# Kernel optimization log

Hardware: AMD Instinct MI355X
Metric: run time of the kernel (lower is better)

Reference implementation:

```python
import jax, jax.numpy as jnp
import numpy as np

N = 50000
E = 800000
C_IN, C_HID, C_OUT = 128, 64, 1


def setup_inputs() -> dict:
    key = jax.random.key(0)
    ks = jax.random.split(key, 8)
    x = jax.random.normal(ks[0], (N, C_IN), dtype=jnp.float32)
    edge_index = jax.random.randint(ks[1], (2, E), 0, N, dtype=jnp.int64)
    # GCNConv linear params (glorot-ish scaling)
    W1 = jax.random.normal(ks[2], (C_IN, C_HID), dtype=jnp.float32) / np.sqrt(C_IN)
    b1 = jnp.zeros((C_HID,), dtype=jnp.float32)
    W2 = jax.random.normal(ks[3], (C_HID, C_HID), dtype=jnp.float32) / np.sqrt(C_HID)
    b2 = jnp.zeros((C_HID,), dtype=jnp.float32)
    W3 = jax.random.normal(ks[4], (C_HID, C_OUT), dtype=jnp.float32) / np.sqrt(C_HID)
    b3 = jnp.zeros((C_OUT,), dtype=jnp.float32)
    return {"x": x, "edge_index": edge_index, "W1": W1, "b1": b1,
            "W2": W2, "b2": b2, "W3": W3, "b3": b3}


def _gcn_norm(edge_index, num_nodes):
    # Add self-loops, compute symmetric normalization D^{-1/2} A D^{-1/2}
    loop = jnp.arange(num_nodes, dtype=edge_index.dtype)
    src = jnp.concatenate([edge_index[0], loop])  # message sources
    dst = jnp.concatenate([edge_index[1], loop])  # message targets
    ones = jnp.ones(src.shape[0], dtype=jnp.float32)
    deg = jax.ops.segment_sum(ones, dst, num_segments=num_nodes)
    dis = jnp.where(deg > 0, jax.lax.rsqrt(jnp.maximum(deg, 1.0)), 0.0)
    norm = dis[src] * dis[dst]  # [E+N]
    return src, dst, norm


def _gcn_conv(h, src, dst, norm, W, b, num_nodes):
    h = h @ W                                  # [N, C_out]
    msg = h[src] * norm[:, None]               # gather + scale, [E+N, C_out]
    out = jax.ops.segment_sum(msg, dst, num_segments=num_nodes)  # scatter-add
    return out + b


def reference(x, edge_index, W1, b1, W2, b2, W3, b3):
    num_nodes = x.shape[0]
    src, dst, norm = _gcn_norm(edge_index, num_nodes)
    leaky = lambda v: jnp.where(v >= 0, v, 0.01 * v)
    h = _gcn_conv(x, src, dst, norm, W1, b1, num_nodes)
    h = leaky(h)
    h = _gcn_conv(h, src, dst, norm, W2, b2, num_nodes)
    h = leaky(h)
    h = _gcn_conv(h, src, dst, norm, W3, b3, num_nodes)
    return h
```

## Files before the change

kernel.cpp:

```cpp
#include <hip/hip_runtime.h>

#define CIN 128
#define CHID 64
#define CSTRIDE 64

__device__ __forceinline__ float leaky(float v) { return v >= 0.f ? v : 0.01f * v; }
__device__ __forceinline__ float bcast(float v, int k) {
    return __int_as_float(__builtin_amdgcn_readlane(__float_as_int(v), k));
}
__device__ __forceinline__ void acc4(float4& a, const float4 v) {
    a.x += v.x; a.y += v.y; a.z += v.z; a.w += v.w;
}
__device__ __forceinline__ void xorred(float4& a) {
    a.x += __shfl_xor(a.x, 16, 64); a.y += __shfl_xor(a.y, 16, 64);
    a.z += __shfl_xor(a.z, 16, 64); a.w += __shfl_xor(a.w, 16, 64);
    a.x += __shfl_xor(a.x, 32, 64); a.y += __shfl_xor(a.y, 32, 64);
    a.z += __shfl_xor(a.z, 32, 64); a.w += __shfl_xor(a.w, 32, 64);
}

__global__ void k_deg(const int* __restrict__ dst, const int* __restrict__ src,
                      int* __restrict__ deg, unsigned short* __restrict__ csr,
                      int E, int nps, int N) {
    const int shard = blockIdx.x & 7;
    const int chunk = blockIdx.x >> 3;
    const int nchunks = gridDim.x >> 3;
    const int lo = shard * nps;
    const int hi = min(lo + nps, N);
    const int estride = nchunks * 256;
    for (int e = chunk * 256 + threadIdx.x; e < E; e += estride) {
        int d = dst[e];
        if (d >= lo && d < hi) {
            int slot = atomicAdd(&deg[d], 1);
            if (slot < CSTRIDE) csr[(d << 6) + slot] = (unsigned short)src[e];
        }
    }
}

__global__ __launch_bounds__(256) void k_gemm1(
    const float* __restrict__ x, const float* __restrict__ W,
    const int* __restrict__ deg, float* __restrict__ hp, int N) {
    const int wave = threadIdx.x >> 6, lane = threadIdx.x & 63;
    float w[CIN];
#pragma unroll
    for (int k = 0; k < CIN; ++k) w[k] = W[k * CHID + lane];
    const int stride = gridDim.x * 4;
    for (int n = blockIdx.x * 4 + wave; n < N; n += stride) {
        float x0 = x[(size_t)n * CIN + lane];
        float x1 = x[(size_t)n * CIN + 64 + lane];
        float acc0 = 0.f, acc1 = 0.f;
#pragma unroll
        for (int k = 0; k < 64; k += 2) {
            acc0 = fmaf(bcast(x0, k),     w[k],     acc0);
            acc1 = fmaf(bcast(x0, k + 1), w[k + 1], acc1);
        }
#pragma unroll
        for (int k = 0; k < 64; k += 2) {
            acc0 = fmaf(bcast(x1, k),     w[64 + k],     acc0);
            acc1 = fmaf(bcast(x1, k + 1), w[64 + k + 1], acc1);
        }
        float dn = rsqrtf((float)(deg[n] + 1));
        hp[(size_t)n * CHID + lane] = dn * (acc0 + acc1);
    }
}

__global__ __launch_bounds__(256) void kG1(
    const unsigned short* __restrict__ csr, const int* __restrict__ deg,
    const float* __restrict__ hp, const float* __restrict__ W2,
    const float* __restrict__ b1, float* __restrict__ hp2, int N) {
    const int wave = threadIdx.x >> 6, lane = threadIdx.x & 63;
    const int g = lane >> 4, sl = lane & 15;
    float w[CHID];
#pragma unroll
    for (int k = 0; k < CHID; ++k) w[k] = W2[k * CHID + lane];
    const float4 bb = ((const float4*)b1)[sl];
    const float4* __restrict__ hpq = (const float4*)hp;
    const int stride = gridDim.x * 4;
    const int n0 = blockIdx.x * 4 + wave;
    int d = 0, c0 = 0, c1 = 0, c2 = 0, c3 = 0;
    if (n0 < N) {
        d = deg[n0];
        int base = n0 << 6;
        c0 = csr[base + g];      c1 = csr[base + g + 4];
        c2 = csr[base + g + 8];  c3 = csr[base + g + 12];
    }
    for (int n = n0; n < N; n += stride) {
        const int n2 = n + stride;
        int dN = 0, e0 = 0, e1 = 0, e2 = 0, e3 = 0;
        if (n2 < N) {
            dN = deg[n2];
            int b2 = n2 << 6;
            e0 = csr[b2 + g];      e1 = csr[b2 + g + 4];
            e2 = csr[b2 + g + 8];  e3 = csr[b2 + g + 12];
        }
        const int dc = d, base = n << 6;
        float4 a0 = make_float4(0.f, 0.f, 0.f, 0.f), a1 = a0, a2 = a0, a3 = a0;
        if (g == 0) a0 = hpq[(size_t)n * 16 + sl];
        if (g < dc)      acc4(a0, hpq[(size_t)c0 * 16 + sl]);
        if (g + 4 < dc)  acc4(a1, hpq[(size_t)c1 * 16 + sl]);
        if (g + 8 < dc)  acc4(a2, hpq[(size_t)c2 * 16 + sl]);
        if (g + 12 < dc) acc4(a3, hpq[(size_t)c3 * 16 + sl]);
        for (int b = g + 16; b < dc; b += 16) {
            { int s = csr[base + b];      acc4(a0, hpq[(size_t)s * 16 + sl]); }
            if (b + 4 < dc)  { int s = csr[base + b + 4];  acc4(a1, hpq[(size_t)s * 16 + sl]); }
            if (b + 8 < dc)  { int s = csr[base + b + 8];  acc4(a2, hpq[(size_t)s * 16 + sl]); }
            if (b + 12 < dc) { int s = csr[base + b + 12]; acc4(a3, hpq[(size_t)s * 16 + sl]); }
        }
        acc4(a0, a1); acc4(a2, a3); acc4(a0, a2);
        xorred(a0);
        float dn = rsqrtf((float)(dc + 1));
        float4 gv;
        gv.x = leaky(dn * a0.x + bb.x);
        gv.y = leaky(dn * a0.y + bb.y);
        gv.z = leaky(dn * a0.z + bb.z);
        gv.w = leaky(dn * a0.w + bb.w);
        float acc0 = 0.f, acc1 = 0.f;
#pragma unroll
        for (int i = 0; i < 16; ++i) {
            acc0 = fmaf(bcast(gv.x, i), w[4 * i + 0], acc0);
            acc1 = fmaf(bcast(gv.y, i), w[4 * i + 1], acc1);
            acc0 = fmaf(bcast(gv.z, i), w[4 * i + 2], acc0);
            acc1 = fmaf(bcast(gv.w, i), w[4 * i + 3], acc1);
        }
        hp2[(size_t)n * CHID + lane] = dn * (acc0 + acc1);
        d = dN; c0 = e0; c1 = e1; c2 = e2; c3 = e3;
    }
}

__global__ __launch_bounds__(256) void kG2(
    const unsigned short* __restrict__ csr, const int* __restrict__ deg,
    const float* __restrict__ hp, const float* __restrict__ b2,
    const float* __restrict__ W3, float* __restrict__ hp3, int N) {
    const int wave = threadIdx.x >> 6, lane = threadIdx.x & 63;
    const int g = lane >> 4, sl = lane & 15;
    const float4 bb = ((const float4*)b2)[sl];
    const float4 w3 = ((const float4*)W3)[sl];
    const float4* __restrict__ hpq = (const float4*)hp;
    const int stride = gridDim.x * 4;
    const int n0 = blockIdx.x * 4 + wave;
    int d = 0, c0 = 0, c1 = 0, c2 = 0, c3 = 0;
    if (n0 < N) {
        d = deg[n0];
        int base = n0 << 6;
        c0 = csr[base + g];      c1 = csr[base + g + 4];
        c2 = csr[base + g + 8];  c3 = csr[base + g + 12];
    }
    for (int n = n0; n < N; n += stride) {
        const int n2 = n + stride;
        int dN = 0, e0 = 0, e1 = 0, e2 = 0, e3 = 0;
        if (n2 < N) {
            dN = deg[n2];
            int b2i = n2 << 6;
            e0 = csr[b2i + g];      e1 = csr[b2i + g + 4];
            e2 = csr[b2i + g + 8];  e3 = csr[b2i + g + 12];
        }
        const int dc = d, base = n << 6;
        float4 a0 = make_float4(0.f, 0.f, 0.f, 0.f), a1 = a0, a2 = a0, a3 = a0;
        if (g == 0) a0 = hpq[(size_t)n * 16 + sl];
        if (g < dc)      acc4(a0, hpq[(size_t)c0 * 16 + sl]);
        if (g + 4 < dc)  acc4(a1, hpq[(size_t)c1 * 16 + sl]);
        if (g + 8 < dc)  acc4(a2, hpq[(size_t)c2 * 16 + sl]);
        if (g + 12 < dc) acc4(a3, hpq[(size_t)c3 * 16 + sl]);
        for (int b = g + 16; b < dc; b += 16) {
            { int s = csr[base + b];      acc4(a0, hpq[(size_t)s * 16 + sl]); }
            if (b + 4 < dc)  { int s = csr[base + b + 4];  acc4(a1, hpq[(size_t)s * 16 + sl]); }
            if (b + 8 < dc)  { int s = csr[base + b + 8];  acc4(a2, hpq[(size_t)s * 16 + sl]); }
            if (b + 12 < dc) { int s = csr[base + b + 12]; acc4(a3, hpq[(size_t)s * 16 + sl]); }
        }
        acc4(a0, a1); acc4(a2, a3); acc4(a0, a2);
        xorred(a0);
        float dn = rsqrtf((float)(dc + 1));
        float t = leaky(dn * a0.x + bb.x) * w3.x
                + leaky(dn * a0.y + bb.y) * w3.y
                + leaky(dn * a0.z + bb.z) * w3.z
                + leaky(dn * a0.w + bb.w) * w3.w;
        t += __shfl_xor(t, 1, 64); t += __shfl_xor(t, 2, 64);
        t += __shfl_xor(t, 4, 64); t += __shfl_xor(t, 8, 64);
        if (lane == 0) hp3[n] = dn * t;
        d = dN; c0 = e0; c1 = e1; c2 = e2; c3 = e3;
    }
}

__global__ void kG3(const unsigned short* __restrict__ csr, const int* __restrict__ deg,
                    const float* __restrict__ hp3, const float* __restrict__ b3,
                    float* __restrict__ out, int N) {
    int t = blockIdx.x * 256 + threadIdx.x;
    int node = t >> 4, sl = t & 15;
    if (node >= N) return;
    int d = deg[node], base = node << 6;
    float acc = (sl == 0) ? hp3[node] : 0.f;
    for (int i = sl; i < d; i += 16) acc += hp3[(int)csr[base + i]];
#pragma unroll
    for (int off = 8; off > 0; off >>= 1) acc += __shfl_down(acc, off, 16);
    if (sl == 0) out[node] = rsqrtf((float)(d + 1)) * acc + b3[0];
}

extern "C" void kernel_launch(void* const* d_in, const int* in_sizes, int n_in,
                              void* d_out, int out_size, void* d_ws, size_t ws_size,
                              hipStream_t stream) {
    const float* x  = (const float*)d_in[0];
    const int*   ei = (const int*)d_in[1];
    const float* W1 = (const float*)d_in[2];
    const float* b1 = (const float*)d_in[3];
    const float* W2 = (const float*)d_in[4];
    const float* b2 = (const float*)d_in[5];
    const float* W3 = (const float*)d_in[6];
    const float* b3 = (const float*)d_in[7];

    const int N = in_sizes[0] / CIN;
    const int E = in_sizes[1] / 2;
    const int* src = ei;
    const int* dst = ei + E;
    const int nps = (N + 7) / 8;

    char* w = (char*)d_ws;
    auto take = [&](size_t bytes) { char* p = w; w += (bytes + 255) & ~(size_t)255; return p; };
    int*            deg = (int*)take((size_t)N * 4);
    unsigned short* csr = (unsigned short*)take((size_t)N * CSTRIDE * 2);
    float*          A   = (float*)take((size_t)N * CHID * 4);
    float*          B   = (float*)take((size_t)N * CHID * 4);
    float*          hp3 = (float*)take((size_t)N * 4);

    hipMemsetAsync(deg, 0, (size_t)N * 4, stream);

    k_deg  <<<2048, 256, 0, stream>>>(dst, src, deg, csr, E, nps, N);
    k_gemm1<<<1024, 256, 0, stream>>>(x, W1, deg, A, N);
    kG1    <<<2048, 256, 0, stream>>>(csr, deg, A, W2, b1, B, N);
    kG2    <<<2048, 256, 0, stream>>>(csr, deg, B, b2, W3, hp3, N);
    kG3    <<<(N * 16 + 255) / 256, 256, 0, stream>>>(csr, deg, hp3, b3, (float*)d_out, N);
}
```

Baseline: 222.9 us.

## Store hidden features in fp16 and gather 8 neighbors per wave

The intermediate hidden feature buffers are stored as fp16 instead of fp32, which halves the bytes moved by each random neighbor-row gather. The gather kernels are restructured so each wave handles 8 neighbors at a time, with each lane loading 16 bytes (8 halves) per row. Accumulation and the reductions stay in fp32. The trade-off is lower precision in the stored intermediates. The neighbor loops are also clamped to the CSR slot capacity, which fixes reads past the fixed-stride CSR when a node's degree exceeds it.

```diff
diff --git a/kernel.cpp b/kernel.cpp
--- a/kernel.cpp
+++ b/kernel.cpp
@@ -1,4 +1,5 @@
 #include <hip/hip_runtime.h>
+#include <hip/hip_fp16.h>
 
 #define CIN 128
 #define CHID 64
@@ -8,14 +9,13 @@
 __device__ __forceinline__ float bcast(float v, int k) {
     return __int_as_float(__builtin_amdgcn_readlane(__float_as_int(v), k));
 }
-__device__ __forceinline__ void acc4(float4& a, const float4 v) {
-    a.x += v.x; a.y += v.y; a.z += v.z; a.w += v.w;
-}
-__device__ __forceinline__ void xorred(float4& a) {
-    a.x += __shfl_xor(a.x, 16, 64); a.y += __shfl_xor(a.y, 16, 64);
-    a.z += __shfl_xor(a.z, 16, 64); a.w += __shfl_xor(a.w, 16, 64);
-    a.x += __shfl_xor(a.x, 32, 64); a.y += __shfl_xor(a.y, 32, 64);
-    a.z += __shfl_xor(a.z, 32, 64); a.w += __shfl_xor(a.w, 32, 64);
+
+__device__ __forceinline__ void accrow(float* a, uint4 u) {
+    float2 f;
+    f = __half22float2(*(__half2*)&u.x); a[0] += f.x; a[1] += f.y;
+    f = __half22float2(*(__half2*)&u.y); a[2] += f.x; a[3] += f.y;
+    f = __half22float2(*(__half2*)&u.z); a[4] += f.x; a[5] += f.y;
+    f = __half22float2(*(__half2*)&u.w); a[6] += f.x; a[7] += f.y;
 }
 
 __global__ void k_deg(const int* __restrict__ dst, const int* __restrict__ src,
@@ -38,7 +38,7 @@
 
 __global__ __launch_bounds__(256) void k_gemm1(
     const float* __restrict__ x, const float* __restrict__ W,
-    const int* __restrict__ deg, float* __restrict__ hp, int N) {
+    const int* __restrict__ deg, __half* __restrict__ hp, int N) {
     const int wave = threadIdx.x >> 6, lane = threadIdx.x & 63;
     float w[CIN];
 #pragma unroll
@@ -59,122 +59,141 @@
             acc1 = fmaf(bcast(x1, k + 1), w[64 + k + 1], acc1);
         }
         float dn = rsqrtf((float)(deg[n] + 1));
-        hp[(size_t)n * CHID + lane] = dn * (acc0 + acc1);
+        hp[(size_t)n * CHID + lane] = __float2half(dn * (acc0 + acc1));
     }
 }
 
 __global__ __launch_bounds__(256) void kG1(
     const unsigned short* __restrict__ csr, const int* __restrict__ deg,
-    const float* __restrict__ hp, const float* __restrict__ W2,
-    const float* __restrict__ b1, float* __restrict__ hp2, int N) {
+    const __half* __restrict__ hp, const float* __restrict__ W2,
+    const float* __restrict__ b1, __half* __restrict__ hp2, int N) {
     const int wave = threadIdx.x >> 6, lane = threadIdx.x & 63;
-    const int g = lane >> 4, sl = lane & 15;
+    const int g = lane >> 3, sub = lane & 7;
     float w[CHID];
 #pragma unroll
     for (int k = 0; k < CHID; ++k) w[k] = W2[k * CHID + lane];
-    const float4 bb = ((const float4*)b1)[sl];
-    const float4* __restrict__ hpq = (const float4*)hp;
+    float bb[8];
+#pragma unroll
+    for (int j = 0; j < 8; ++j) bb[j] = b1[8 * sub + j];
+    const uint4* __restrict__ hpq = (const uint4*)hp;
     const int stride = gridDim.x * 4;
     const int n0 = blockIdx.x * 4 + wave;
+
     int d = 0, c0 = 0, c1 = 0, c2 = 0, c3 = 0;
     if (n0 < N) {
         d = deg[n0];
-        int base = n0 << 6;
-        c0 = csr[base + g];      c1 = csr[base + g + 4];
-        c2 = csr[base + g + 8];  c3 = csr[base + g + 12];
-    }
+        const int base = n0 << 6;
+        c0 = csr[base + g];      c1 = csr[base + g + 8];
+        c2 = csr[base + g + 16]; c3 = csr[base + g + 24];
+    }
+
     for (int n = n0; n < N; n += stride) {
         const int n2 = n + stride;
         int dN = 0, e0 = 0, e1 = 0, e2 = 0, e3 = 0;
         if (n2 < N) {
             dN = deg[n2];
-            int b2 = n2 << 6;
-            e0 = csr[b2 + g];      e1 = csr[b2 + g + 4];
-            e2 = csr[b2 + g + 8];  e3 = csr[b2 + g + 12];
-        }
-        const int dc = d, base = n << 6;
-        float4 a0 = make_float4(0.f, 0.f, 0.f, 0.f), a1 = a0, a2 = a0, a3 = a0;
-        if (g == 0) a0 = hpq[(size_t)n * 16 + sl];
-        if (g < dc)      acc4(a0, hpq[(size_t)c0 * 16 + sl]);
-        if (g + 4 < dc)  acc4(a1, hpq[(size_t)c1 * 16 + sl]);
-        if (g + 8 < dc)  acc4(a2, hpq[(size_t)c2 * 16 + sl]);
-        if (g + 12 < dc) acc4(a3, hpq[(size_t)c3 * 16 + sl]);
-        for (int b = g + 16; b < dc; b += 16) {
-            { int s = csr[base + b];      acc4(a0, hpq[(size_t)s * 16 + sl]); }
-            if (b + 4 < dc)  { int s = csr[base + b + 4];  acc4(a1, hpq[(size_t)s * 16 + sl]); }
-            if (b + 8 < dc)  { int s = csr[base + b + 8];  acc4(a2, hpq[(size_t)s * 16 + sl]); }
-            if (b + 12 < dc) { int s = csr[base + b + 12]; acc4(a3, hpq[(size_t)s * 16 + sl]); }
-        }
-        acc4(a0, a1); acc4(a2, a3); acc4(a0, a2);
-        xorred(a0);
-        float dn = rsqrtf((float)(dc + 1));
-        float4 gv;
-        gv.x = leaky(dn * a0.x + bb.x);
-        gv.y = leaky(dn * a0.y + bb.y);
-        gv.z = leaky(dn * a0.z + bb.z);
-        gv.w = leaky(dn * a0.w + bb.w);
-        float acc0 = 0.f, acc1 = 0.f;
-#pragma unroll
-        for (int i = 0; i < 16; ++i) {
-            acc0 = fmaf(bcast(gv.x, i), w[4 * i + 0], acc0);
-            acc1 = fmaf(bcast(gv.y, i), w[4 * i + 1], acc1);
-            acc0 = fmaf(bcast(gv.z, i), w[4 * i + 2], acc0);
-            acc1 = fmaf(bcast(gv.w, i), w[4 * i + 3], acc1);
-        }
-        hp2[(size_t)n * CHID + lane] = dn * (acc0 + acc1);
+            const int b2i = n2 << 6;
+            e0 = csr[b2i + g];      e1 = csr[b2i + g + 8];
+            e2 = csr[b2i + g + 16]; e3 = csr[b2i + g + 24];
+        }
+        const int dcur = d;
+        const int dc = min(dcur, CSTRIDE);
+        float a0[8] = {0,0,0,0,0,0,0,0}, a1[8] = {0,0,0,0,0,0,0,0};
+        if (g == 0)      accrow(a0, hpq[(size_t)n  * 8 + sub]);
+        if (g < dc)      accrow(a0, hpq[(size_t)c0 * 8 + sub]);
+        if (g + 8 < dc)  accrow(a1, hpq[(size_t)c1 * 8 + sub]);
+        if (g + 16 < dc) accrow(a0, hpq[(size_t)c2 * 8 + sub]);
+        if (g + 24 < dc) accrow(a1, hpq[(size_t)c3 * 8 + sub]);
+        if (dc > 32) {
+            const int base = n << 6;
+            for (int b = g + 32; b < dc; b += 8) {
+                int s = csr[base + b];
+                accrow(a0, hpq[(size_t)s * 8 + sub]);
+            }
+        }
+#pragma unroll
+        for (int j = 0; j < 8; ++j) a0[j] += a1[j];
+#pragma unroll
+        for (int j = 0; j < 8; ++j) a0[j] += __shfl_xor(a0[j], 8, 64);
+#pragma unroll
+        for (int j = 0; j < 8; ++j) a0[j] += __shfl_xor(a0[j], 16, 64);
+#pragma unroll
+        for (int j = 0; j < 8; ++j) a0[j] += __shfl_xor(a0[j], 32, 64);
+        float dn = rsqrtf((float)(dcur + 1));
+        float gv[8];
+#pragma unroll
+        for (int j = 0; j < 8; ++j) gv[j] = leaky(dn * a0[j] + bb[j]);
+        float acc0 = 0.f, acc1 = 0.f, acc2 = 0.f, acc3 = 0.f;
+#pragma unroll
+        for (int c = 0; c < 64; c += 4) {
+            acc0 = fmaf(bcast(gv[(c + 0) & 7], (c + 0) >> 3), w[c + 0], acc0);
+            acc1 = fmaf(bcast(gv[(c + 1) & 7], (c + 1) >> 3), w[c + 1], acc1);
+            acc2 = fmaf(bcast(gv[(c + 2) & 7], (c + 2) >> 3), w[c + 2], acc2);
+            acc3 = fmaf(bcast(gv[(c + 3) & 7], (c + 3) >> 3), w[c + 3], acc3);
+        }
+        hp2[(size_t)n * CHID + lane] = __float2half(dn * ((acc0 + acc1) + (acc2 + acc3)));
         d = dN; c0 = e0; c1 = e1; c2 = e2; c3 = e3;
     }
 }
 
 __global__ __launch_bounds__(256) void kG2(
     const unsigned short* __restrict__ csr, const int* __restrict__ deg,
-    const float* __restrict__ hp, const float* __restrict__ b2,
+    const __half* __restrict__ hp, const float* __restrict__ b2,
     const float* __restrict__ W3, float* __restrict__ hp3, int N) {
     const int wave = threadIdx.x >> 6, lane = threadIdx.x & 63;
-    const int g = lane >> 4, sl = lane & 15;
-    const float4 bb = ((const float4*)b2)[sl];
-    const float4 w3 = ((const float4*)W3)[sl];
-    const float4* __restrict__ hpq = (const float4*)hp;
+    const int g = lane >> 3, sub = lane & 7;
+    float bb[8], w3v[8];
+#pragma unroll
+    for (int j = 0; j < 8; ++j) { bb[j] = b2[8 * sub + j]; w3v[j] = W3[8 * sub + j]; }
+    const uint4* __restrict__ hpq = (const uint4*)hp;
     const int stride = gridDim.x * 4;
     const int n0 = blockIdx.x * 4 + wave;
+
     int d = 0, c0 = 0, c1 = 0, c2 = 0, c3 = 0;
     if (n0 < N) {
         d = deg[n0];
-        int base = n0 << 6;
-        c0 = csr[base + g];      c1 = csr[base + g + 4];
-        c2 = csr[base + g + 8];  c3 = csr[base + g + 12];
-    }
+        const int base = n0 << 6;
+        c0 = csr[base + g];      c1 = csr[base + g + 8];
+        c2 = csr[base + g + 16]; c3 = csr[base + g + 24];
+    }
+
     for (int n = n0; n < N; n += stride) {
         const int n2 = n + stride;
         int dN = 0, e0 = 0, e1 = 0, e2 = 0, e3 = 0;
         if (n2 < N) {
             dN = deg[n2];
-            int b2i = n2 << 6;
-            e0 = csr[b2i + g];      e1 = csr[b2i + g + 4];
-            e2 = csr[b2i + g + 8];  e3 = csr[b2i + g + 12];
-        }
-        const int dc = d, base = n << 6;
-        float4 a0 = make_float4(0.f, 0.f, 0.f, 0.f), a1 = a0, a2 = a0, a3 = a0;
-        if (g == 0) a0 = hpq[(size_t)n * 16 + sl];
-        if (g < dc)      acc4(a0, hpq[(size_t)c0 * 16 + sl]);
-        if (g + 4 < dc)  acc4(a1, hpq[(size_t)c1 * 16 + sl]);
-        if (g + 8 < dc)  acc4(a2, hpq[(size_t)c2 * 16 + sl]);
-        if (g + 12 < dc) acc4(a3, hpq[(size_t)c3 * 16 + sl]);
-        for (int b = g + 16; b < dc; b += 16) {
-            { int s = csr[base + b];      acc4(a0, hpq[(size_t)s * 16 + sl]); }
-            if (b + 4 < dc)  { int s = csr[base + b + 4];  acc4(a1, hpq[(size_t)s * 16 + sl]); }
-            if (b + 8 < dc)  { int s = csr[base + b + 8];  acc4(a2, hpq[(size_t)s * 16 + sl]); }
-            if (b + 12 < dc) { int s = csr[base + b + 12]; acc4(a3, hpq[(size_t)s * 16 + sl]); }
-        }
-        acc4(a0, a1); acc4(a2, a3); acc4(a0, a2);
-        xorred(a0);
-        float dn = rsqrtf((float)(dc + 1));
-        float t = leaky(dn * a0.x + bb.x) * w3.x
-                + leaky(dn * a0.y + bb.y) * w3.y
-                + leaky(dn * a0.z + bb.z) * w3.z
-                + leaky(dn * a0.w + bb.w) * w3.w;
-        t += __shfl_xor(t, 1, 64); t += __shfl_xor(t, 2, 64);
-        t += __shfl_xor(t, 4, 64); t += __shfl_xor(t, 8, 64);
+            const int b2i = n2 << 6;
+            e0 = csr[b2i + g];      e1 = csr[b2i + g + 8];
+            e2 = csr[b2i + g + 16]; e3 = csr[b2i + g + 24];
+        }
+        const int dcur = d;
+        const int dc = min(dcur, CSTRIDE);
+        float a0[8] = {0,0,0,0,0,0,0,0}, a1[8] = {0,0,0,0,0,0,0,0};
+        if (g == 0)      accrow(a0, hpq[(size_t)n  * 8 + sub]);
+        if (g < dc)      accrow(a0, hpq[(size_t)c0 * 8 + sub]);
+        if (g + 8 < dc)  accrow(a1, hpq[(size_t)c1 * 8 + sub]);
+        if (g + 16 < dc) accrow(a0, hpq[(size_t)c2 * 8 + sub]);
+        if (g + 24 < dc) accrow(a1, hpq[(size_t)c3 * 8 + sub]);
+        if (dc > 32) {
+            const int base = n << 6;
+            for (int b = g + 32; b < dc; b += 8) {
+                int s = csr[base + b];
+                accrow(a0, hpq[(size_t)s * 8 + sub]);
+            }
+        }
+#pragma unroll
+        for (int j = 0; j < 8; ++j) a0[j] += a1[j];
+#pragma unroll
+        for (int j = 0; j < 8; ++j) a0[j] += __shfl_xor(a0[j], 8, 64);
+#pragma unroll
+        for (int j = 0; j < 8; ++j) a0[j] += __shfl_xor(a0[j], 16, 64);
+#pragma unroll
+        for (int j = 0; j < 8; ++j) a0[j] += __shfl_xor(a0[j], 32, 64);
+        float dn = rsqrtf((float)(dcur + 1));
+        float t = 0.f;
+#pragma unroll
+        for (int j = 0; j < 8; ++j) t = fmaf(leaky(dn * a0[j] + bb[j]), w3v[j], t);
+        t += __shfl_xor(t, 1, 64); t += __shfl_xor(t, 2, 64); t += __shfl_xor(t, 4, 64);
         if (lane == 0) hp3[n] = dn * t;
         d = dN; c0 = e0; c1 = e1; c2 = e2; c3 = e3;
     }
@@ -187,8 +206,9 @@
     int node = t >> 4, sl = t & 15;
     if (node >= N) return;
     int d = deg[node], base = node << 6;
+    int dl = min(d, CSTRIDE);
     float acc = (sl == 0) ? hp3[node] : 0.f;
-    for (int i = sl; i < d; i += 16) acc += hp3[(int)csr[base + i]];
+    for (int i = sl; i < dl; i += 16) acc += hp3[(int)csr[base + i]];
 #pragma unroll
     for (int off = 8; off > 0; off >>= 1) acc += __shfl_down(acc, off, 16);
     if (sl == 0) out[node] = rsqrtf((float)(d + 1)) * acc + b3[0];
@@ -216,8 +236,8 @@
     auto take = [&](size_t bytes) { char* p = w; w += (bytes + 255) & ~(size_t)255; return p; };
     int*            deg = (int*)take((size_t)N * 4);
     unsigned short* csr = (unsigned short*)take((size_t)N * CSTRIDE * 2);
-    float*          A   = (float*)take((size_t)N * CHID * 4);
-    float*          B   = (float*)take((size_t)N * CHID * 4);
+    __half*         A   = (__half*)take((size_t)N * CHID * 2);
+    __half*         B   = (__half*)take((size_t)N * CHID * 2);
     float*          hp3 = (float*)take((size_t)N * 4);
 
     hipMemsetAsync(deg, 0, (size_t)N * 4, stream);
```

Measured after the change: 228.6 us. +2.6%, slower.
